# Optimization experiments

Measured on AMD Instinct MI355X. Metric: run time of the kernel, lower is better.

The kernel has to match this reference:

```python
import jax, jax.numpy as jnp
import numpy as np

K = 4  # hard-coded in ParticleNet.__init__

# (fan_in, fan_out) for all linear layers
_DIMS = [(10, 32), (32, 64),        # edgeconv1 MLP (2*5 -> 32 -> 64)
         (128, 96), (96, 128),      # edgeconv2 MLP (2*64 -> 96 -> 128)
         (256, 192), (192, 256),    # edgeconv3 MLP (2*128 -> 192 -> 256)
         (453, 453), (453, 226), (226, 2)]  # output head (5+64+128+256=453)
_PNAMES = ['c1w1', 'c1w2', 'c2w1', 'c2w2', 'c3w1', 'c3w2', 'ow1', 'ow2', 'ow3']


def setup_inputs() -> dict:
    key = jax.random.key(0)
    ks = jax.random.split(key, 2 + len(_DIMS))
    inp = {
        'coords': jax.random.normal(ks[0], (1024, 128, 2), dtype=jnp.float32),
        'features': jax.random.normal(ks[1], (1024, 128, 5), dtype=jnp.float32),
    }
    for i, (name, (fi, fo)) in enumerate(zip(_PNAMES, _DIMS)):
        inp[name] = jax.random.normal(ks[2 + i], (fi, fo), dtype=jnp.float32) / np.sqrt(fi)
        inp[name.replace('w', 'b')] = jnp.zeros((fo,), dtype=jnp.float32)
    return inp


def _knn_idx(x, k):
    # x: [B,N,C] -> idx of k nearest neighbors (excluding self): [B,N,k]
    x2 = jnp.sum(x * x, axis=-1)                              # [B,N]
    d = x2[:, :, None] + x2[:, None, :] - 2.0 * jnp.einsum('bnc,bmc->bnm', x, x)
    d = d + jnp.eye(x.shape[1], dtype=x.dtype) * 1e9          # no self-loops
    _, idx = jax.lax.top_k(-d, k)
    return idx


def _edgeconv(x, idx, w1, b1, w2, b2):
    # EdgeConv: message = MLP([x_i, x_j - x_i]), mean-aggregated over k neighbors
    xj = jax.vmap(lambda xb, ib: xb[ib])(x, idx)              # [B,N,k,C]
    xi = jnp.broadcast_to(x[:, :, None, :], xj.shape)
    h = jnp.concatenate([xi, xj - xi], axis=-1)               # [B,N,k,2C]
    h = jax.nn.elu(h @ w1 + b1)
    h = jax.nn.elu(h @ w2 + b2)
    return jnp.mean(h, axis=2)                                # [B,N,out]


def reference(coords, features, c1w1, c1b1, c1w2, c1b2, c2w1, c2b1, c2w2, c2b2,
              c3w1, c3b1, c3w2, c3b2, ow1, ob1, ow2, ob2, ow3, ob3):
    idx1 = _knn_idx(coords, K)
    out1 = _edgeconv(features, idx1, c1w1, c1b1, c1w2, c1b2)  # [B,N,64]
    idx2 = _knn_idx(out1, K)
    out2 = _edgeconv(out1, idx2, c2w1, c2b1, c2w2, c2b2)      # [B,N,128]
    idx3 = _knn_idx(out2, K)
    out3 = _edgeconv(out2, idx3, c3w1, c3b1, c3w2, c3b2)      # [B,N,256]
    h = jnp.concatenate([features, out1, out2, out3], axis=-1)  # [B,N,453]
    h = jax.nn.elu(h @ ow1 + ob1)
    h = jax.nn.elu(h @ ow2 + ob2)
    return h @ ow3 + ob3                                      # [B,N,2]
```

## Files before the change

kernel.cpp:

```cpp
#include <hip/hip_runtime.h>
#include <cstdint>
#include <cstddef>


#define NB 1024
#define NPT 128

typedef __attribute__((ext_vector_type(8))) short short8;
typedef __attribute__((ext_vector_type(4))) float floatx4;
typedef __attribute__((ext_vector_type(4))) unsigned int uint4v;

__device__ __forceinline__ float elu_f(float x) { return x > 0.0f ? x : expm1f(x); }

__device__ __forceinline__ unsigned short f2bf(float f) {
  unsigned u = __builtin_bit_cast(unsigned, f);
  unsigned r = u + 0x7FFFu + ((u >> 16) & 1u);
  return (unsigned short)(r >> 16);
}
__device__ __forceinline__ float bf2f(unsigned short h) {
  unsigned u = ((unsigned)h) << 16;
  return __builtin_bit_cast(float, u);
}

template<int C>
__global__ __launch_bounds__(128) void knn_kernel(const float* __restrict__ x,
                                                  int* __restrict__ idx) {
  __shared__ __align__(16) float xs[NPT][C + 4];
  __shared__ float x2s[NPT];
  __shared__ double x2d[NPT];
  const int b = blockIdx.x, t = threadIdx.x;
  const float* xb = x + (size_t)b * NPT * C;
  for (int e = t; e < NPT * C; e += 128) xs[e / C][e % C] = xb[e];
  __syncthreads();
  float xi[C];
  float s2 = 0.0f;
  double s2d = 0.0;
#pragma unroll
  for (int c = 0; c < C; ++c) {
    xi[c] = xs[t][c];
    s2 += xi[c] * xi[c];
    s2d += (double)xi[c] * (double)xi[c];
  }
  x2s[t] = s2;
  x2d[t] = s2d;
  __syncthreads();
  float bd0 = 1e30f, bd1 = 1e30f, bd2 = 1e30f, bd3 = 1e30f, bd4 = 1e30f, bd5 = 1e30f;
  int bi0 = 0, bi1 = 0, bi2 = 0, bi3 = 0, bi4 = 0, bi5 = 0;
  for (int j = 0; j < NPT; ++j) {
    if (j == t) continue;
    float dot = 0.0f;
#pragma unroll
    for (int c = 0; c < C; ++c) dot += xi[c] * xs[j][c];
    float d = s2 + x2s[j] - 2.0f * dot;
    if (d < bd5) {
      bd5 = d; bi5 = j;
      if (bd5 < bd4) {
        float td = bd4; bd4 = bd5; bd5 = td; int ti = bi4; bi4 = bi5; bi5 = ti;
        if (bd4 < bd3) {
          td = bd3; bd3 = bd4; bd4 = td; ti = bi3; bi3 = bi4; bi4 = ti;
          if (bd3 < bd2) {
            td = bd2; bd2 = bd3; bd3 = td; ti = bi2; bi2 = bi3; bi3 = ti;
            if (bd2 < bd1) {
              td = bd1; bd1 = bd2; bd2 = td; ti = bi1; bi1 = bi2; bi2 = ti;
              if (bd1 < bd0) {
                td = bd0; bd0 = bd1; bd1 = td; ti = bi0; bi0 = bi1; bi1 = ti;
              }
            }
          }
        }
      }
    }
  }
  auto refine = [&](int j) -> double {
    double dot = 0.0;
#pragma unroll
    for (int c = 0; c < C; ++c) dot += (double)xi[c] * (double)xs[j][c];
    return s2d + x2d[j] - 2.0 * dot;
  };
  double e0 = refine(bi0), e1 = refine(bi1), e2 = refine(bi2);
  double e3 = refine(bi3), e4 = refine(bi4), e5 = refine(bi5);
#define CSWP(da, ia, db, ib)                                            \
  if ((da > db) || (da == db && ia > ib)) {                             \
    double _td = da; da = db; db = _td; int _ti = ia; ia = ib; ib = _ti; }
  CSWP(e0, bi0, e1, bi1) CSWP(e1, bi1, e2, bi2) CSWP(e2, bi2, e3, bi3)
  CSWP(e3, bi3, e4, bi4) CSWP(e4, bi4, e5, bi5)
  CSWP(e0, bi0, e1, bi1) CSWP(e1, bi1, e2, bi2) CSWP(e2, bi2, e3, bi3)
  CSWP(e3, bi3, e4, bi4)
  CSWP(e0, bi0, e1, bi1) CSWP(e1, bi1, e2, bi2) CSWP(e2, bi2, e3, bi3)
  CSWP(e0, bi0, e1, bi1) CSWP(e1, bi1, e2, bi2)
  CSWP(e0, bi0, e1, bi1)
#undef CSWP
  int* ib = idx + ((size_t)b * NPT + t) * 4;
  ib[0] = bi0; ib[1] = bi1; ib[2] = bi2; ib[3] = bi3;
}

template<int C>
__global__ __launch_bounds__(512) void knn512_kernel(const float* __restrict__ x,
                                                     int* __restrict__ idx) {
  constexpr int CQ = C / 4;
  constexpr int QS = CQ + 4;
  __shared__ __align__(16) float xs[NPT][4 * QS];
  __shared__ float x2s[NPT];
  __shared__ double x2d[NPT];
  const int b = blockIdx.x, t = threadIdx.x;
  const float* xb = x + (size_t)b * NPT * C;
  for (int e = t; e < NPT * C; e += 512) {
    int r = e / C, c = e % C;
    xs[r][(c / CQ) * QS + (c % CQ)] = xb[e];
  }
  __syncthreads();
  const int p = t >> 2, q = t & 3;
  float xi[CQ];
  float s2 = 0.f;
  double s2d = 0.0;
#pragma unroll
  for (int c = 0; c < CQ; ++c) {
    xi[c] = xs[p][q * QS + c];
    s2 += xi[c] * xi[c];
    s2d += (double)xi[c] * (double)xi[c];
  }
  s2 += __shfl_xor(s2, 1);  s2 += __shfl_xor(s2, 2);
  s2d += __shfl_xor(s2d, 1); s2d += __shfl_xor(s2d, 2);
  if (q == 0) { x2s[p] = s2; x2d[p] = s2d; }
  __syncthreads();
  float bd0 = 1e30f, bd1 = 1e30f, bd2 = 1e30f, bd3 = 1e30f, bd4 = 1e30f, bd5 = 1e30f;
  int bi0 = 0, bi1 = 0, bi2 = 0, bi3 = 0, bi4 = 0, bi5 = 0;
  for (int j = 0; j < NPT; ++j) {
    if (j == p) continue;
    const float4* xr = reinterpret_cast<const float4*>(&xs[j][q * QS]);
    float part0 = 0.f, part1 = 0.f, part2 = 0.f, part3 = 0.f;
#pragma unroll
    for (int c4 = 0; c4 < CQ / 4; ++c4) {
      float4 v = xr[c4];
      float s = xi[4 * c4 + 0] * v.x + xi[4 * c4 + 1] * v.y +
                xi[4 * c4 + 2] * v.z + xi[4 * c4 + 3] * v.w;
      if ((c4 & 3) == 0) part0 += s;
      else if ((c4 & 3) == 1) part1 += s;
      else if ((c4 & 3) == 2) part2 += s;
      else part3 += s;
    }
    float dot = (part0 + part1) + (part2 + part3);
    dot += __shfl_xor(dot, 1);
    dot += __shfl_xor(dot, 2);
    float d = s2 + x2s[j] - 2.0f * dot;
    if (d < bd5) {
      bd5 = d; bi5 = j;
      if (bd5 < bd4) {
        float td = bd4; bd4 = bd5; bd5 = td; int ti = bi4; bi4 = bi5; bi5 = ti;
        if (bd4 < bd3) {
          td = bd3; bd3 = bd4; bd4 = td; ti = bi3; bi3 = bi4; bi4 = ti;
          if (bd3 < bd2) {
            td = bd2; bd2 = bd3; bd3 = td; ti = bi2; bi2 = bi3; bi3 = ti;
            if (bd2 < bd1) {
              td = bd1; bd1 = bd2; bd2 = td; ti = bi1; bi1 = bi2; bi2 = ti;
              if (bd1 < bd0) {
                td = bd0; bd0 = bd1; bd1 = td; ti = bi0; bi0 = bi1; bi1 = ti;
              }
            }
          }
        }
      }
    }
  }
  auto refine = [&](int j) -> double {
    double dot = 0.0;
#pragma unroll
    for (int c = 0; c < CQ; ++c) dot += (double)xi[c] * (double)xs[j][q * QS + c];
    dot += __shfl_xor(dot, 1);
    dot += __shfl_xor(dot, 2);
    return s2d + x2d[j] - 2.0 * dot;
  };
  double e0 = refine(bi0), e1 = refine(bi1), e2 = refine(bi2);
  double e3 = refine(bi3), e4 = refine(bi4), e5 = refine(bi5);
#define CSWP(da, ia, db, ib)                                            \
  if ((da > db) || (da == db && ia > ib)) {                             \
    double _td = da; da = db; db = _td; int _ti = ia; ia = ib; ib = _ti; }
  CSWP(e0, bi0, e1, bi1) CSWP(e1, bi1, e2, bi2) CSWP(e2, bi2, e3, bi3)
  CSWP(e3, bi3, e4, bi4) CSWP(e4, bi4, e5, bi5)
  CSWP(e0, bi0, e1, bi1) CSWP(e1, bi1, e2, bi2) CSWP(e2, bi2, e3, bi3)
  CSWP(e3, bi3, e4, bi4)
  CSWP(e0, bi0, e1, bi1) CSWP(e1, bi1, e2, bi2) CSWP(e2, bi2, e3, bi3)
  CSWP(e0, bi0, e1, bi1) CSWP(e1, bi1, e2, bi2)
  CSWP(e0, bi0, e1, bi1)
#undef CSWP
  if (q == 0) {
    int* ib = idx + ((size_t)b * NPT + p) * 4;
    ib[0] = bi0; ib[1] = bi1; ib[2] = bi2; ib[3] = bi3;
  }
}

__global__ __launch_bounds__(256) void ec1_kernel(
    const float* __restrict__ feat, const int* __restrict__ idx,
    const float* __restrict__ w1, const float* __restrict__ b1,
    const float* __restrict__ w2, const float* __restrict__ b2,
    float* __restrict__ out) {
  __shared__ __align__(16) float fs[NPT][6];
  __shared__ __align__(16) float w1s[10][32];
  __shared__ __align__(16) float w2s[32][68];
  __shared__ float hs[256][33];
  __shared__ float b1s[32], b2s[64];
  const int z = blockIdx.x, t = threadIdx.x;
  const int b = z >> 1, hh = z & 1;
  const float* fb = feat + (size_t)b * NPT * 5;
  for (int e = t; e < NPT * 5; e += 256) fs[e / 5][e % 5] = fb[e];
  for (int e = t; e < 320; e += 256) w1s[e / 32][e % 32] = w1[e];
  for (int e = t; e < 2048; e += 256) w2s[e >> 6][e & 63] = w2[e];
  if (t < 32) b1s[t] = b1[t];
  if (t >= 192) b2s[t - 192] = b2[t - 192];
  __syncthreads();
  {
    const int p = hh * 64 + (t >> 2);
    const int j = idx[(size_t)b * 512 + p * 4 + (t & 3)];
    float h[32];
#pragma unroll
    for (int o = 0; o < 32; ++o) h[o] = b1s[o];
#pragma unroll
    for (int c = 0; c < 10; ++c) {
      float in_c = (c < 5) ? fs[p][c] : (fs[j][c - 5] - fs[p][c - 5]);
      const float4* wr = reinterpret_cast<const float4*>(&w1s[c][0]);
#pragma unroll
      for (int o4 = 0; o4 < 8; ++o4) {
        float4 w = wr[o4];
        h[4 * o4 + 0] += in_c * w.x; h[4 * o4 + 1] += in_c * w.y;
        h[4 * o4 + 2] += in_c * w.z; h[4 * o4 + 3] += in_c * w.w;
      }
    }
#pragma unroll
    for (int o = 0; o < 32; ++o) hs[t][o] = elu_f(h[o]);
  }
  __syncthreads();
  {
    const int g = t >> 2, q = t & 3;
    const int o0 = q * 16;
    float acc[4][16];
#pragma unroll
    for (int m = 0; m < 16; ++m) {
      float bv = b2s[o0 + m];
#pragma unroll
      for (int i = 0; i < 4; ++i) acc[i][m] = bv;
    }
    for (int k = 0; k < 32; ++k) {
      float hk0 = hs[g * 4 + 0][k];
      float hk1 = hs[g * 4 + 1][k];
      float hk2 = hs[g * 4 + 2][k];
      float hk3 = hs[g * 4 + 3][k];
      const float4* wr = reinterpret_cast<const float4*>(&w2s[k][o0]);
#pragma unroll
      for (int m4 = 0; m4 < 4; ++m4) {
        float4 w = wr[m4];
        acc[0][4 * m4 + 0] += hk0 * w.x; acc[0][4 * m4 + 1] += hk0 * w.y;
        acc[0][4 * m4 + 2] += hk0 * w.z; acc[0][4 * m4 + 3] += hk0 * w.w;
        acc[1][4 * m4 + 0] += hk1 * w.x; acc[1][4 * m4 + 1] += hk1 * w.y;
        acc[1][4 * m4 + 2] += hk1 * w.z; acc[1][4 * m4 + 3] += hk1 * w.w;
        acc[2][4 * m4 + 0] += hk2 * w.x; acc[2][4 * m4 + 1] += hk2 * w.y;
        acc[2][4 * m4 + 2] += hk2 * w.z; acc[2][4 * m4 + 3] += hk2 * w.w;
        acc[3][4 * m4 + 0] += hk3 * w.x; acc[3][4 * m4 + 1] += hk3 * w.y;
        acc[3][4 * m4 + 2] += hk3 * w.z; acc[3][4 * m4 + 3] += hk3 * w.w;
      }
    }
    float* ob = out + ((size_t)b * NPT + hh * 64 + g) * 64 + o0;
#pragma unroll
    for (int m4 = 0; m4 < 4; ++m4) {
      float4 v;
      float* vp = &v.x;
#pragma unroll
      for (int s = 0; s < 4; ++s) {
        int m = 4 * m4 + s;
        vp[s] = 0.25f * (elu_f(acc[0][m]) + elu_f(acc[1][m]) +
                         elu_f(acc[2][m]) + elu_f(acc[3][m]));
      }
      *reinterpret_cast<float4*>(&ob[4 * m4]) = v;
    }
  }
}

__global__ __launch_bounds__(512, 2) void ec2a_kernel(
    const float* __restrict__ x, const int* __restrict__ idx,
    const float* __restrict__ w1, const float* __restrict__ b1,
    float* __restrict__ H) {
  __shared__ __align__(16) float xs[NPT][68];
  __shared__ __align__(16) float w1s[128][100];
  __shared__ float b1s[96];
  const int b = blockIdx.x, t = threadIdx.x;
  const float* xb = x + (size_t)b * NPT * 64;
  for (int e = t; e < NPT * 64; e += 512) xs[e >> 6][e & 63] = xb[e];
  for (int e = t; e < 128 * 96; e += 512) w1s[e / 96][e % 96] = w1[e];
  if (t < 96) b1s[t] = b1[t];
  __syncthreads();
  const int pb = t >> 2, part = t & 3;
  const int n0 = part * 24;
  int jn[4];
#pragma unroll
  for (int i = 0; i < 4; ++i) jn[i] = idx[(size_t)b * 512 + pb * 4 + i];
  float acc[4][24];
#pragma unroll
  for (int m = 0; m < 24; ++m) {
    float bv = b1s[n0 + m];
#pragma unroll
    for (int i = 0; i < 4; ++i) acc[i][m] = bv;
  }
  for (int c = 0; c < 64; ++c) {
    float in_c = xs[pb][c];
    const float4* wr = reinterpret_cast<const float4*>(&w1s[c][n0]);
#pragma unroll
    for (int q4 = 0; q4 < 6; ++q4) {
      float4 wv = wr[q4];
#pragma unroll
      for (int i = 0; i < 4; ++i) {
        acc[i][4 * q4 + 0] += in_c * wv.x;
        acc[i][4 * q4 + 1] += in_c * wv.y;
        acc[i][4 * q4 + 2] += in_c * wv.z;
        acc[i][4 * q4 + 3] += in_c * wv.w;
      }
    }
  }
  for (int c = 0; c < 64; ++c) {
    float xic = xs[pb][c];
    float in0 = xs[jn[0]][c] - xic;
    float in1 = xs[jn[1]][c] - xic;
    float in2 = xs[jn[2]][c] - xic;
    float in3 = xs[jn[3]][c] - xic;
    const float4* wr = reinterpret_cast<const float4*>(&w1s[64 + c][n0]);
#pragma unroll
    for (int q4 = 0; q4 < 6; ++q4) {
      float4 wv = wr[q4];
      acc[0][4 * q4 + 0] += in0 * wv.x; acc[0][4 * q4 + 1] += in0 * wv.y;
      acc[0][4 * q4 + 2] += in0 * wv.z; acc[0][4 * q4 + 3] += in0 * wv.w;
      acc[1][4 * q4 + 0] += in1 * wv.x; acc[1][4 * q4 + 1] += in1 * wv.y;
      acc[1][4 * q4 + 2] += in1 * wv.z; acc[1][4 * q4 + 3] += in1 * wv.w;
      acc[2][4 * q4 + 0] += in2 * wv.x; acc[2][4 * q4 + 1] += in2 * wv.y;
      acc[2][4 * q4 + 2] += in2 * wv.z; acc[2][4 * q4 + 3] += in2 * wv.w;
      acc[3][4 * q4 + 0] += in3 * wv.x; acc[3][4 * q4 + 1] += in3 * wv.y;
      acc[3][4 * q4 + 2] += in3 * wv.z; acc[3][4 * q4 + 3] += in3 * wv.w;
    }
  }
#pragma unroll
  for (int i = 0; i < 4; ++i) {
    float* hrow = H + ((size_t)b * 512 + pb * 4 + i) * 96 + n0;
#pragma unroll
    for (int q4 = 0; q4 < 6; ++q4) {
      float4 v = {elu_f(acc[i][4 * q4 + 0]), elu_f(acc[i][4 * q4 + 1]),
                  elu_f(acc[i][4 * q4 + 2]), elu_f(acc[i][4 * q4 + 3])};
      *reinterpret_cast<float4*>(&hrow[4 * q4]) = v;
    }
  }
}

__global__ __launch_bounds__(512, 2) void ec2b_kernel(
    const float* __restrict__ H, const float* __restrict__ w2,
    const float* __restrict__ b2, float* __restrict__ out) {
  __shared__ __align__(16) float hsT[96][260];
  __shared__ float w2s[96][132];
  __shared__ float b2s[128];
  const int z = blockIdx.x, t = threadIdx.x;
  const int bc = z >> 1, hh = z & 1;
  const float* Hb = H + ((size_t)bc * 512 + hh * 256) * 96;
  for (int i = t; i < 256 * 96; i += 512) hsT[i % 96][i / 96] = Hb[i];
  for (int i = t; i < 96 * 128; i += 512) w2s[i >> 7][i & 127] = w2[i];
  if (t < 128) b2s[t] = b2[t];
  __syncthreads();
  const int g = t >> 3, oq = t & 7;
  float acc[4][16];
#pragma unroll
  for (int m = 0; m < 16; ++m) {
    float bv = b2s[oq + 8 * m];
#pragma unroll
    for (int i = 0; i < 4; ++i) acc[i][m] = bv;
  }
  for (int k = 0; k < 96; ++k) {
    float4 hv = *reinterpret_cast<const float4*>(&hsT[k][4 * g]);
#pragma unroll
    for (int m = 0; m < 16; ++m) {
      float wv = w2s[k][oq + 8 * m];
      acc[0][m] += hv.x * wv;
      acc[1][m] += hv.y * wv;
      acc[2][m] += hv.z * wv;
      acc[3][m] += hv.w * wv;
    }
  }
  float* orow = out + ((size_t)bc * NPT + hh * 64 + g) * 128;
#pragma unroll
  for (int m = 0; m < 16; ++m) {
    float s = elu_f(acc[0][m]) + elu_f(acc[1][m]) +
              elu_f(acc[2][m]) + elu_f(acc[3][m]);
    orow[oq + 8 * m] = 0.25f * s;
  }
}

__global__ __launch_bounds__(512, 2) void ec3a_kernel(
    const float* __restrict__ x, const int* __restrict__ idx,
    const float* __restrict__ w1, const float* __restrict__ b1,
    unsigned short* __restrict__ h1) {
  __shared__ unsigned short Xb[128][136];
  __shared__ unsigned short W1t[192][264];
  __shared__ float b1s[192];
  __shared__ unsigned short stg[8][16][40];
  const int b = blockIdx.x, t = threadIdx.x;
  const float* xb = x + (size_t)b * NPT * 128;
  for (int e = t; e < NPT * 128; e += 512) Xb[e >> 7][e & 127] = f2bf(xb[e]);
  for (int e = t; e < 256 * 192; e += 512) {
    int k = e / 192, n = e % 192;
    W1t[n][k] = f2bf(w1[e]);
  }
  if (t < 192) b1s[t] = b1[t];
  __syncthreads();
  const int w = t >> 6, l = t & 63;
  const int lr = l & 15, lq = l >> 4;
  for (int mt = 0; mt < 4; ++mt) {
    const int m = (w * 4 + mt) * 16;
    const int e = m + lr;
    const int p = e >> 2;
    const int jp = idx[(size_t)b * 512 + e];
    short8 A[8];
#pragma unroll
    for (int kk = 0; kk < 4; ++kk) {
      int k0 = kk * 32 + lq * 8;
      A[kk] = *reinterpret_cast<const short8*>(&Xb[p][k0]);
    }
#pragma unroll
    for (int kk = 0; kk < 4; ++kk) {
      int k0 = kk * 32 + lq * 8;
      short8 aj = *reinterpret_cast<const short8*>(&Xb[jp][k0]);
      short8 ai = *reinterpret_cast<const short8*>(&Xb[p][k0]);
      short8 d;
#pragma unroll
      for (int q = 0; q < 8; ++q)
        d[q] = (short)f2bf(bf2f((unsigned short)aj[q]) - bf2f((unsigned short)ai[q]));
      A[4 + kk] = d;
    }
    floatx4 acc[12];
#pragma unroll
    for (int n = 0; n < 12; ++n) acc[n] = (floatx4){0.f, 0.f, 0.f, 0.f};
#pragma unroll
    for (int n = 0; n < 12; ++n) {
#pragma unroll
      for (int kk = 0; kk < 8; ++kk) {
        short8 Bf = *reinterpret_cast<const short8*>(&W1t[n * 16 + lr][kk * 32 + lq * 8]);
        acc[n] = __builtin_amdgcn_mfma_f32_16x16x32_bf16(A[kk], Bf, acc[n], 0, 0, 0);
      }
    }
#pragma unroll
    for (int pr = 0; pr < 6; ++pr) {
      float bv0 = b1s[pr * 32 + lr];
      float bv1 = b1s[pr * 32 + 16 + lr];
#pragma unroll
      for (int i = 0; i < 4; ++i) {
        stg[w][lq * 4 + i][lr]      = f2bf(elu_f(acc[2 * pr][i] + bv0));
        stg[w][lq * 4 + i][16 + lr] = f2bf(elu_f(acc[2 * pr + 1][i] + bv1));
      }
      asm volatile("s_waitcnt lgkmcnt(0)" ::: "memory");
      const unsigned short* src = &stg[w][l >> 2][(l & 3) * 8];
      uint4v vv = *reinterpret_cast<const uint4v*>(src);
      size_t dst = ((size_t)b * 512 + m + (l >> 2)) * 192 + pr * 32 + (l & 3) * 8;
      *reinterpret_cast<uint4v*>(&h1[dst]) = vv;
      asm volatile("s_waitcnt lgkmcnt(0)" ::: "memory");
    }
  }
}

__global__ __launch_bounds__(512, 2) void ec3b_kernel(
    const unsigned short* __restrict__ h1,
    const float* __restrict__ w2, const float* __restrict__ b2,
    unsigned short* __restrict__ out3) {
  __shared__ unsigned short W2t[256][200];
  __shared__ float b2s[256];
  const int b = blockIdx.x, t = threadIdx.x;
  for (int e = t; e < 192 * 256; e += 512) {
    int k = e >> 8, n = e & 255;
    W2t[n][k] = f2bf(w2[e]);
  }
  if (t < 256) b2s[t] = b2[t];
  __syncthreads();
  const int w = t >> 6, l = t & 63;
  const int lr = l & 15, lq = l >> 4;
  for (int mt = 0; mt < 4; ++mt) {
    const int m = (w * 4 + mt) * 16;
    floatx4 acc[16];
#pragma unroll
    for (int n = 0; n < 16; ++n) acc[n] = (floatx4){0.f, 0.f, 0.f, 0.f};
    const unsigned short* arow = h1 + ((size_t)b * 512 + m + lr) * 192;
#pragma unroll
    for (int kk = 0; kk < 6; ++kk) {
      short8 Af = *reinterpret_cast<const short8*>(&arow[kk * 32 + lq * 8]);
#pragma unroll
      for (int n = 0; n < 16; ++n) {
        short8 Bf = *reinterpret_cast<const short8*>(&W2t[n * 16 + lr][kk * 32 + lq * 8]);
        acc[n] = __builtin_amdgcn_mfma_f32_16x16x32_bf16(Af, Bf, acc[n], 0, 0, 0);
      }
    }
    unsigned short* orow = out3 + ((size_t)b * NPT + (m >> 2) + lq) * 256;
#pragma unroll
    for (int n = 0; n < 16; ++n) {
      float bv = b2s[n * 16 + lr];
      float s = 0.f;
#pragma unroll
      for (int i = 0; i < 4; ++i) s += elu_f(acc[n][i] + bv);
      orow[n * 16 + lr] = f2bf(0.25f * s);
    }
  }
}

__global__ __launch_bounds__(256) void head_prep_kernel(
    const float* __restrict__ w1, const float* __restrict__ w2,
    unsigned short* __restrict__ w1p, unsigned short* __restrict__ w2p) {
  int i = blockIdx.x * 256 + threadIdx.x;
  if (i < 512 * 480) {
    int n = i / 480, kp = i % 480;
    int ko = (kp < 5) ? kp : kp - 3;
    bool ok = ((kp < 5) || (kp >= 8 && kp < 456)) && (n < 453);
    w1p[i] = ok ? f2bf(w1[(size_t)ko * 453 + n]) : (unsigned short)0;
  } else {
    int j = i - 512 * 480;
    if (j < 256 * 480) {
      int n = j / 480, kp = j % 480;
      bool ok = (kp < 453) && (n < 226);
      w2p[j] = ok ? f2bf(w2[(size_t)kp * 226 + n]) : (unsigned short)0;
    }
  }
}

#define HSTR 488
__global__ __launch_bounds__(256) void head_mfma_kernel(
    const float* __restrict__ feat, const float* __restrict__ o1,
    const float* __restrict__ o2, const unsigned short* __restrict__ o3,
    const unsigned short* __restrict__ w1p, const float* __restrict__ b1,
    const unsigned short* __restrict__ w2p, const float* __restrict__ b2,
    const float* __restrict__ w3, const float* __restrict__ b3,
    float* __restrict__ out) {
  __shared__ unsigned short uA[64 * HSTR];
  __shared__ unsigned short uH[64 * HSTR];
  __shared__ float b1s[512], b2s[256], w3s[512];
  const int t = threadIdx.x;
  const size_t base = (size_t)blockIdx.x * 64;

  for (int e = t; e < 64 * 8; e += 256) {
    int r = e >> 3, c = e & 7;
    uA[r * HSTR + c] = (c < 5) ? f2bf(feat[(base + r) * 5 + c]) : 0;
  }
  for (int e = t; e < 64 * 64; e += 256) {
    int r = e >> 6, c = e & 63;
    uA[r * HSTR + 8 + c] = f2bf(o1[(base + r) * 64 + c]);
  }
  for (int e = t; e < 64 * 128; e += 256) {
    int r = e >> 7, c = e & 127;
    uA[r * HSTR + 72 + c] = f2bf(o2[(base + r) * 128 + c]);
  }
  for (int e = t; e < 64 * 256; e += 256) {
    int r = e >> 8, c = e & 255;
    uA[r * HSTR + 200 + c] = o3[(base + r) * 256 + c];
  }
  for (int e = t; e < 64 * 32; e += 256) {
    int r = e >> 5, c = e & 31;
    uA[r * HSTR + 456 + c] = 0;
  }
  for (int i = t; i < 512; i += 256) b1s[i] = (i < 453) ? b1[i] : 0.f;
  if (t < 256) b2s[t] = (t < 226) ? b2[t] : 0.f;
  for (int i = t; i < 512; i += 256) w3s[i] = (i < 452) ? w3[i] : 0.f;
  __syncthreads();

  const int w = t >> 6, l = t & 63;
  const int lr = l & 15, lq = l >> 4;
  const int tr = t >> 2, tc = t & 3;

  short8 Af[15];
#pragma unroll
  for (int kk = 0; kk < 15; ++kk)
    Af[kk] = *reinterpret_cast<const short8*>(
        &uA[(w * 16 + lr) * HSTR + kk * 32 + lq * 8]);
  __syncthreads();

  uint4v v[15];
#define WLOAD(SRC, CH)                                                   \
  {                                                                      \
    _Pragma("unroll")                                                    \
    for (int i = 0; i < 15; ++i)                                         \
      v[i] = *reinterpret_cast<const uint4v*>(                           \
          &SRC[((size_t)((CH) * 64 + tr)) * 480 + (tc + 4 * i) * 8]);    \
  }
#define WWRITE()                                                         \
  {                                                                      \
    _Pragma("unroll")                                                    \
    for (int i = 0; i < 15; ++i)                                         \
      *reinterpret_cast<uint4v*>(&uA[tr * HSTR + (tc + 4 * i) * 8]) = v[i]; \
  }

  WLOAD(w1p, 0)
  WWRITE()
  __syncthreads();

  for (int ch = 0; ch < 8; ++ch) {
    if (ch < 7) WLOAD(w1p, ch + 1)
    floatx4 a0 = {0.f, 0.f, 0.f, 0.f}, a1 = {0.f, 0.f, 0.f, 0.f};
    floatx4 a2 = {0.f, 0.f, 0.f, 0.f}, a3 = {0.f, 0.f, 0.f, 0.f};
#pragma unroll
    for (int kk = 0; kk < 15; ++kk) {
      int ko = kk * 32 + lq * 8;
      short8 B0 = *reinterpret_cast<const short8*>(&uA[(lr)*HSTR + ko]);
      short8 B1 = *reinterpret_cast<const short8*>(&uA[(16 + lr) * HSTR + ko]);
      short8 B2 = *reinterpret_cast<const short8*>(&uA[(32 + lr) * HSTR + ko]);
      short8 B3 = *reinterpret_cast<const short8*>(&uA[(48 + lr) * HSTR + ko]);
      a0 = __builtin_amdgcn_mfma_f32_16x16x32_bf16(Af[kk], B0, a0, 0, 0, 0);
      a1 = __builtin_amdgcn_mfma_f32_16x16x32_bf16(Af[kk], B1, a1, 0, 0, 0);
      a2 = __builtin_amdgcn_mfma_f32_16x16x32_bf16(Af[kk], B2, a2, 0, 0, 0);
      a3 = __builtin_amdgcn_mfma_f32_16x16x32_bf16(Af[kk], B3, a3, 0, 0, 0);
    }
    {
      floatx4 aj[4] = {a0, a1, a2, a3};
#pragma unroll
      for (int jx = 0; jx < 4; ++jx) {
        int c = ch * 64 + jx * 16 + lr;
        if (c < 480) {
          float bb = b1s[c];
#pragma unroll
          for (int i = 0; i < 4; ++i) {
            int row = w * 16 + lq * 4 + i;
            uH[row * HSTR + c] =
                (c < 453) ? f2bf(elu_f(aj[jx][i] + bb)) : (unsigned short)0;
          }
        }
      }
    }
    __syncthreads();
    if (ch < 7) WWRITE()
    __syncthreads();
  }

#pragma unroll
  for (int kk = 0; kk < 15; ++kk)
    Af[kk] = *reinterpret_cast<const short8*>(
        &uH[(w * 16 + lr) * HSTR + kk * 32 + lq * 8]);
  WLOAD(w2p, 0)
  WWRITE()
  __syncthreads();

  float p0[4] = {0.f, 0.f, 0.f, 0.f}, p1[4] = {0.f, 0.f, 0.f, 0.f};
  for (int ch = 0; ch < 4; ++ch) {
    if (ch < 3) WLOAD(w2p, ch + 1)
    floatx4 a0 = {0.f, 0.f, 0.f, 0.f}, a1 = {0.f, 0.f, 0.f, 0.f};
    floatx4 a2 = {0.f, 0.f, 0.f, 0.f}, a3 = {0.f, 0.f, 0.f, 0.f};
#pragma unroll
    for (int kk = 0; kk < 15; ++kk) {
      int ko = kk * 32 + lq * 8;
      short8 B0 = *reinterpret_cast<const short8*>(&uA[(lr)*HSTR + ko]);
      short8 B1 = *reinterpret_cast<const short8*>(&uA[(16 + lr) * HSTR + ko]);
      short8 B2 = *reinterpret_cast<const short8*>(&uA[(32 + lr) * HSTR + ko]);
      short8 B3 = *reinterpret_cast<const short8*>(&uA[(48 + lr) * HSTR + ko]);
      a0 = __builtin_amdgcn_mfma_f32_16x16x32_bf16(Af[kk], B0, a0, 0, 0, 0);
      a1 = __builtin_amdgcn_mfma_f32_16x16x32_bf16(Af[kk], B1, a1, 0, 0, 0);
      a2 = __builtin_amdgcn_mfma_f32_16x16x32_bf16(Af[kk], B2, a2, 0, 0, 0);
      a3 = __builtin_amdgcn_mfma_f32_16x16x32_bf16(Af[kk], B3, a3, 0, 0, 0);
    }
    {
      floatx4 aj[4] = {a0, a1, a2, a3};
#pragma unroll
      for (int jx = 0; jx < 4; ++jx) {
        int c = ch * 64 + jx * 16 + lr;
        float bb = b2s[c];
        float wa = w3s[2 * c], wb = w3s[2 * c + 1];
#pragma unroll
        for (int i = 0; i < 4; ++i) {
          float h = (c < 226) ? elu_f(aj[jx][i] + bb) : 0.f;
          p0[i] += h * wa;
          p1[i] += h * wb;
        }
      }
    }
    __syncthreads();
    if (ch < 3) WWRITE()
    __syncthreads();
  }

#pragma unroll
  for (int i = 0; i < 4; ++i) {
    float a = p0[i], bvv = p1[i];
#pragma unroll
    for (int m = 1; m < 16; m <<= 1) {
      a += __shfl_xor(a, m);
      bvv += __shfl_xor(bvv, m);
    }
    if (lr == 0) {
      size_t row = base + w * 16 + lq * 4 + i;
      float2 vv = {a + b3[0], bvv + b3[1]};
      *reinterpret_cast<float2*>(&out[row * 2]) = vv;
    }
  }
#undef WLOAD
#undef WWRITE
}

extern "C" void kernel_launch(void* const* d_in, const int* in_sizes, int n_in,
                              void* d_out, int out_size, void* d_ws, size_t ws_size,
                              hipStream_t stream) {
  const float* coords = (const float*)d_in[0];
  const float* feat   = (const float*)d_in[1];
  const float* c1w1 = (const float*)d_in[2];  const float* c1b1 = (const float*)d_in[3];
  const float* c1w2 = (const float*)d_in[4];  const float* c1b2 = (const float*)d_in[5];
  const float* c2w1 = (const float*)d_in[6];  const float* c2b1 = (const float*)d_in[7];
  const float* c2w2 = (const float*)d_in[8];  const float* c2b2 = (const float*)d_in[9];
  const float* c3w1 = (const float*)d_in[10]; const float* c3b1 = (const float*)d_in[11];
  const float* c3w2 = (const float*)d_in[12]; const float* c3b2 = (const float*)d_in[13];
  const float* ow1  = (const float*)d_in[14]; const float* ob1  = (const float*)d_in[15];
  const float* ow2  = (const float*)d_in[16]; const float* ob2  = (const float*)d_in[17];
  const float* ow3  = (const float*)d_in[18]; const float* ob3  = (const float*)d_in[19];
  float* out = (float*)d_out;

  char* ws = (char*)d_ws;
  float* out1 = (float*)(ws);
  float* out2 = (float*)(ws + (32ull << 20));
  unsigned short* out3b = (unsigned short*)(ws + (96ull << 20));
  int* idx = (int*)(ws + (160ull << 20));
  float* Hbuf = (float*)(ws + (162ull << 20));
  unsigned short* h1 = (unsigned short*)(ws + (162ull << 20));
  unsigned short* w1p = (unsigned short*)(ws + (212ull << 20));
  unsigned short* w2p = (unsigned short*)(ws + (213ull << 20));

  head_prep_kernel<<<1440, 256, 0, stream>>>(ow1, ow2, w1p, w2p);
  knn_kernel<2><<<NB, 128, 0, stream>>>(coords, idx);
  ec1_kernel<<<2 * NB, 256, 0, stream>>>(feat, idx, c1w1, c1b1, c1w2, c1b2, out1);
  knn512_kernel<64><<<NB, 512, 0, stream>>>(out1, idx);
  for (int c = 0; c < 4; ++c) {
    ec2a_kernel<<<256, 512, 0, stream>>>(out1 + (size_t)c * 256 * NPT * 64,
                                         idx + (size_t)c * 256 * 512,
                                         c2w1, c2b1, Hbuf);
    ec2b_kernel<<<512, 512, 0, stream>>>(Hbuf, c2w2, c2b2,
                                         out2 + (size_t)c * 256 * NPT * 128);
  }
  knn512_kernel<128><<<NB, 512, 0, stream>>>(out2, idx);
  for (int c = 0; c < 4; ++c) {
    ec3a_kernel<<<256, 512, 0, stream>>>(out2 + (size_t)c * 256 * NPT * 128,
                                         idx + (size_t)c * 256 * 512,
                                         c3w1, c3b1, h1);
    ec3b_kernel<<<256, 512, 0, stream>>>(h1, c3w2, c3b2,
                                         out3b + (size_t)c * 256 * NPT * 256);
  }
  head_mfma_kernel<<<2048, 256, 0, stream>>>(feat, out1, out2, out3b,
                                             w1p, ob1, w2p, ob2, ow3, ob3, out);
}
```

Baseline: 2.139 ms.

## Keep head layer-1 activations in registers via per-wave transpose scratch, raise occupancy

```diff
diff --git a/kernel.cpp b/kernel.cpp
--- a/kernel.cpp
+++ b/kernel.cpp
@@ -520,7 +520,8 @@
 }
 
 #define HSTR 488
-__global__ __launch_bounds__(256) void head_mfma_kernel(
+#define TPSS 72
+__global__ __launch_bounds__(256, 2) void head_mfma_kernel(
     const float* __restrict__ feat, const float* __restrict__ o1,
     const float* __restrict__ o2, const unsigned short* __restrict__ o3,
     const unsigned short* __restrict__ w1p, const float* __restrict__ b1,
@@ -528,7 +529,7 @@
     const float* __restrict__ w3, const float* __restrict__ b3,
     float* __restrict__ out) {
   __shared__ unsigned short uA[64 * HSTR];
-  __shared__ unsigned short uH[64 * HSTR];
+  __shared__ __align__(16) unsigned short tps[4][16][TPSS];
   __shared__ float b1s[512], b2s[256], w3s[512];
   const int t = threadIdx.x;
   const size_t base = (size_t)blockIdx.x * 64;
@@ -588,8 +589,11 @@
   WWRITE()
   __syncthreads();
 
+  short8 Af2[15];
+#pragma unroll
   for (int ch = 0; ch < 8; ++ch) {
     if (ch < 7) WLOAD(w1p, ch + 1)
+    else       WLOAD(w2p, 0)
     floatx4 a0 = {0.f, 0.f, 0.f, 0.f}, a1 = {0.f, 0.f, 0.f, 0.f};
     floatx4 a2 = {0.f, 0.f, 0.f, 0.f}, a3 = {0.f, 0.f, 0.f, 0.f};
 #pragma unroll
@@ -609,31 +613,24 @@
 #pragma unroll
       for (int jx = 0; jx < 4; ++jx) {
         int c = ch * 64 + jx * 16 + lr;
-        if (c < 480) {
-          float bb = b1s[c];
-#pragma unroll
-          for (int i = 0; i < 4; ++i) {
-            int row = w * 16 + lq * 4 + i;
-            uH[row * HSTR + c] =
-                (c < 453) ? f2bf(elu_f(aj[jx][i] + bb)) : (unsigned short)0;
-          }
-        }
-      }
-    }
+        float bb = b1s[c];
+#pragma unroll
+        for (int i = 0; i < 4; ++i)
+          tps[w][lq * 4 + i][jx * 16 + lr] = f2bf(elu_f(aj[jx][i] + bb));
+      }
+    }
+    asm volatile("s_waitcnt lgkmcnt(0)" ::: "memory");
+    Af2[2 * ch] = *reinterpret_cast<const short8*>(&tps[w][lr][lq * 8]);
+    if (ch < 7)
+      Af2[2 * ch + 1] = *reinterpret_cast<const short8*>(&tps[w][lr][32 + lq * 8]);
+    asm volatile("s_waitcnt lgkmcnt(0)" ::: "memory");
     __syncthreads();
-    if (ch < 7) WWRITE()
+    WWRITE()
     __syncthreads();
   }
 
-#pragma unroll
-  for (int kk = 0; kk < 15; ++kk)
-    Af[kk] = *reinterpret_cast<const short8*>(
-        &uH[(w * 16 + lr) * HSTR + kk * 32 + lq * 8]);
-  WLOAD(w2p, 0)
-  WWRITE()
-  __syncthreads();
-
   float p0[4] = {0.f, 0.f, 0.f, 0.f}, p1[4] = {0.f, 0.f, 0.f, 0.f};
+#pragma unroll
   for (int ch = 0; ch < 4; ++ch) {
     if (ch < 3) WLOAD(w2p, ch + 1)
     floatx4 a0 = {0.f, 0.f, 0.f, 0.f}, a1 = {0.f, 0.f, 0.f, 0.f};
@@ -645,10 +642,10 @@
       short8 B1 = *reinterpret_cast<const short8*>(&uA[(16 + lr) * HSTR + ko]);
       short8 B2 = *reinterpret_cast<const short8*>(&uA[(32 + lr) * HSTR + ko]);
       short8 B3 = *reinterpret_cast<const short8*>(&uA[(48 + lr) * HSTR + ko]);
-      a0 = __builtin_amdgcn_mfma_f32_16x16x32_bf16(Af[kk], B0, a0, 0, 0, 0);
-      a1 = __builtin_amdgcn_mfma_f32_16x16x32_bf16(Af[kk], B1, a1, 0, 0, 0);
-      a2 = __builtin_amdgcn_mfma_f32_16x16x32_bf16(Af[kk], B2, a2, 0, 0, 0);
-      a3 = __builtin_amdgcn_mfma_f32_16x16x32_bf16(Af[kk], B3, a3, 0, 0, 0);
+      a0 = __builtin_amdgcn_mfma_f32_16x16x32_bf16(Af2[kk], B0, a0, 0, 0, 0);
+      a1 = __builtin_amdgcn_mfma_f32_16x16x32_bf16(Af2[kk], B1, a1, 0, 0, 0);
+      a2 = __builtin_amdgcn_mfma_f32_16x16x32_bf16(Af2[kk], B2, a2, 0, 0, 0);
+      a3 = __builtin_amdgcn_mfma_f32_16x16x32_bf16(Af2[kk], B3, a3, 0, 0, 0);
     }
     {
       floatx4 aj[4] = {a0, a1, a2, a3};
@@ -665,9 +662,11 @@
         }
       }
     }
-    __syncthreads();
-    if (ch < 3) WWRITE()
-    __syncthreads();
+    if (ch < 3) {
+      __syncthreads();
+      WWRITE()
+      __syncthreads();
+    }
   }
 
 #pragma unroll
```

After: 2.002 ms. -6.4%, faster.
